# Performance work log

Measured on AMD Instinct MI355X. Metric: run time of the kernel, lower is better.

Reference implementation:

```python
import jax, jax.numpy as jnp
import numpy as np

N, B, H, D = 8, 4, 16, 64   # batch, beam, heads, head_dim
T, S, L = 16, 1024, 1024    # new tokens, prefix len, past len
E = H * D
SCALE = 1.0 / np.sqrt(D).astype(np.float32)


def setup_inputs() -> dict:
    key = jax.random.key(0)
    ks = jax.random.split(key, 10)
    wscale = 1.0 / np.sqrt(E).astype(np.float32)
    return {
        "hidden_states": jax.random.normal(ks[0], (N * B, T, E), jnp.float32),
        "attention_mask": jnp.zeros((N * B, 1, 1, S + L + T), jnp.float32),
        "rel_pos": jax.random.normal(ks[1], (N * B, H, T, S + L + T), jnp.float32) * 0.1,
        "past_prefix_key": jax.random.normal(ks[2], (N, H, S, D), jnp.float32),
        "past_prefix_value": jax.random.normal(ks[3], (N, H, S, D), jnp.float32),
        "past_key": jax.random.normal(ks[4], (N * B, H, L, D), jnp.float32),
        "past_value": jax.random.normal(ks[5], (N * B, H, L, D), jnp.float32),
        "Wq": jax.random.normal(ks[6], (E, E), jnp.float32) * wscale,
        "bq": jnp.zeros((E,), jnp.float32),
        "Wk": jax.random.normal(ks[7], (E, E), jnp.float32) * wscale,
        "bk": jnp.zeros((E,), jnp.float32),
        "Wv": jax.random.normal(ks[8], (E, E), jnp.float32) * wscale,
        "bv": jnp.zeros((E,), jnp.float32),
    }


def _heads(x):
    # (NB, T, E) -> (NB, H, T, D)
    nb, t, _ = x.shape
    return x.reshape(nb, t, H, D).transpose(0, 2, 1, 3)


def reference(hidden_states, attention_mask, rel_pos, past_prefix_key,
              past_prefix_value, past_key, past_value, Wq, bq, Wk, bk, Wv, bv):
    q = _heads(hidden_states @ Wq.T + bq)   # (NB,H,T,D)
    k = _heads(hidden_states @ Wk.T + bk)
    v = _heads(hidden_states @ Wv.T + bv)

    # prefix scores: batch-shared prefix KV, per-beam queries
    q5 = q.reshape(N, B, H, T, D)
    prefix_scores = jnp.einsum('bxhtd,bhsd->bxhts', q5, past_prefix_key)
    prefix_scores = prefix_scores.reshape(N * B, H, T, S) * SCALE

    key_layer = jnp.concatenate([past_key, k], axis=2)      # (NB,H,L+T,D)
    value_layer = jnp.concatenate([past_value, v], axis=2)
    scores = jnp.einsum('bhtd,bhsd->bhts', q, key_layer) * SCALE

    scores = jnp.concatenate([prefix_scores, scores], axis=-1)  # (NB,H,T,S+L+T)
    scores = scores + rel_pos + attention_mask
    probs = jax.nn.softmax(scores, axis=-1)

    prefix_probs = probs[..., :S]
    rest_probs = probs[..., S:]

    prefix_ctx = jnp.einsum('bxhts,bhsd->bxhtd',
                            prefix_probs.reshape(N, B, H, T, S),
                            past_prefix_value).reshape(N * B, H, T, D)
    ctx = prefix_ctx + jnp.einsum('bhts,bhsd->bhtd', rest_probs, value_layer)

    # (NB,H,T,D) -> (NB,T,E)
    return ctx.transpose(0, 2, 1, 3).reshape(N * B, T, E)
```

## Files before the change

kernel.cpp:

```cpp
#include <hip/hip_runtime.h>

#define NH 16
#define NT 16
#define DD 64
#define SS 1024
#define LL 1024
#define TOTK 2064
#define EE 1024
#define NWAVE 8

typedef __attribute__((ext_vector_type(8))) short bf16x8;
typedef __attribute__((ext_vector_type(4))) float f32x4;

__device__ __forceinline__ unsigned short f2bf(float x) {
  union { float f; unsigned u; } v; v.f = x;
  unsigned r = v.u + 0x7fffu + ((v.u >> 16) & 1u);
  return (unsigned short)(r >> 16);
}

__device__ __forceinline__ void dma16(const void* g, void* l) {
  __builtin_amdgcn_global_load_lds(
      (const __attribute__((address_space(1))) unsigned int*)g,
      (__attribute__((address_space(3))) unsigned int*)l, 16, 0, 0);
}

__global__ __launch_bounds__(256)
void proj_kernel(const float* __restrict__ hidden,
                 const float* __restrict__ Wq, const float* __restrict__ bq,
                 const float* __restrict__ Wk, const float* __restrict__ bk,
                 const float* __restrict__ Wv, const float* __restrict__ bv,
                 unsigned short* __restrict__ qws,
                 float* __restrict__ kws, float* __restrict__ vws)
{
  __shared__ alignas(16) unsigned short As[64][72];
  __shared__ alignas(16) unsigned short Bs[64][72];
  const int mtile = blockIdx.x;
  const int ntile = blockIdx.y;
  const int mat = ntile >> 4;
  const int h = ntile & 15;
  const float* Wm = (mat == 0) ? Wq : (mat == 1 ? Wk : Wv);
  const float* bm = (mat == 0) ? bq : (mat == 1 ? bk : bv);
  const int tid = threadIdx.x;
  const int lane = tid & 63, w = tid >> 6;
  const int lr = lane & 15, lg = lane >> 4;
  const int m0 = mtile * 64;

  const f32x4 fz = {0.f, 0.f, 0.f, 0.f};
  f32x4 acc[4];
  #pragma unroll
  for (int j = 0; j < 4; ++j) acc[j] = fz;

  const int srow = tid >> 4, sc4 = tid & 15;
  float4 Ar[4], Br[4];
  #pragma unroll
  for (int it = 0; it < 4; ++it) {
    Ar[it] = *(const float4*)(hidden + (m0 + srow + it * 16) * EE + sc4 * 4);
    Br[it] = *(const float4*)(Wm + (h * 64 + srow + it * 16) * EE + sc4 * 4);
  }

  for (int k0 = 0; k0 < EE; k0 += 64) {
    __syncthreads();
    #pragma unroll
    for (int it = 0; it < 4; ++it) {
      int row = srow + it * 16;
      float4 a = Ar[it], b = Br[it];
      *(ushort4*)(&As[row][sc4 * 4]) = make_ushort4(f2bf(a.x), f2bf(a.y), f2bf(a.z), f2bf(a.w));
      *(ushort4*)(&Bs[row][sc4 * 4]) = make_ushort4(f2bf(b.x), f2bf(b.y), f2bf(b.z), f2bf(b.w));
    }
    __syncthreads();
    int kn = k0 + 64;
    if (kn < EE) {
      #pragma unroll
      for (int it = 0; it < 4; ++it) {
        Ar[it] = *(const float4*)(hidden + (m0 + srow + it * 16) * EE + kn + sc4 * 4);
        Br[it] = *(const float4*)(Wm + (h * 64 + srow + it * 16) * EE + kn + sc4 * 4);
      }
    }
    #pragma unroll
    for (int hh = 0; hh < 2; ++hh) {
      bf16x8 a = *(const bf16x8*)(&As[w * 16 + lr][hh * 32 + lg * 8]);
      #pragma unroll
      for (int dt = 0; dt < 4; ++dt) {
        bf16x8 b = *(const bf16x8*)(&Bs[dt * 16 + lr][hh * 32 + lg * 8]);
        acc[dt] = __builtin_amdgcn_mfma_f32_16x16x32_bf16(a, b, acc[dt], 0, 0, 0);
      }
    }
  }

  #pragma unroll
  for (int dt = 0; dt < 4; ++dt)
    #pragma unroll
    for (int r = 0; r < 4; ++r) {
      int Mrow = m0 + w * 16 + lg * 4 + r;
      int nb = Mrow >> 4, t = Mrow & 15;
      int d = dt * 16 + lr;
      float val = acc[dt][r] + bm[h * 64 + d];
      int oi = ((nb * NH + h) * NT + t) * DD + d;
      if (mat == 0) qws[oi] = f2bf(val);
      else if (mat == 1) kws[oi] = val;
      else vws[oi] = val;
    }
}

__global__ __launch_bounds__(512)
void attn_kernel(const float* __restrict__ mask, const float* __restrict__ rel,
                 const float* __restrict__ ppk, const float* __restrict__ ppv,
                 const float* __restrict__ pk, const float* __restrict__ pv,
                 const unsigned short* __restrict__ qws,
                 const float* __restrict__ kws, const float* __restrict__ vws,
                 float* __restrict__ out)
{
  __shared__ __align__(16) float SB[2 * 2 * 128 * 64];
  __shared__ __align__(16) unsigned short Pb[NWAVE][16][40];

  const int wg = blockIdx.x;
  const int nb = wg >> 4, h = wg & 15;
  const int n = nb >> 2;
  const int tid = threadIdx.x;
  const int lane = tid & 63, w = tid >> 6;
  const int lr = lane & 15, lg = lane >> 4;

  const unsigned short* qbase = qws + ((nb * NH + h) * NT) * DD;
  bf16x8 aq0 = *(const bf16x8*)(qbase + lr * DD + lg * 8);
  bf16x8 aq1 = *(const bf16x8*)(qbase + lr * DD + lg * 8 + 32);

  const float* relbase = rel + ((nb * NH + h) * NT) * TOTK;
  const float* mbase = mask + nb * TOTK;

  if (lane < 32) {
    int t = lane & 15, half = lane >> 4;
    float4 z = {0.f, 0.f, 0.f, 0.f};
    *(float4*)(&Pb[w][t][16 + half * 8]) = z;
  }

  const f32x4 fz = {0.f, 0.f, 0.f, 0.f};
  f32x4 ctx[4];
  float ls[4];
  #pragma unroll
  for (int dt = 0; dt < 4; ++dt) ctx[dt] = fz;
  #pragma unroll
  for (int r = 0; r < 4; ++r) ls[r] = 0.f;

  auto stage = [&](int c, int buf) {
    const float *ks, *vs;
    if (c < 8) {
      int j = c * 128;
      ks = ppk + ((n * NH + h) * SS + j) * DD;
      vs = ppv + ((n * NH + h) * SS + j) * DD;
    } else if (c < 16) {
      int j = (c - 8) * 128;
      ks = pk + ((nb * NH + h) * LL + j) * DD;
      vs = pv + ((nb * NH + h) * LL + j) * DD;
    } else {
      ks = kws + ((nb * NH + h) * NT) * DD;
      vs = vws + ((nb * NH + h) * NT) * DD;
    }
    float* Kb = SB + buf * 2 * 128 * 64;
    float* Vb = Kb + 128 * 64;
    #pragma unroll
    for (int q = 0; q < 4; ++q) {
      int Lrow = w * 16 + q * 4 + (lane >> 4);
      int colb = (lane & 15) * 16;
      int scolb = colb ^ ((Lrow & 7) << 4);
      int srow = (c == 16) ? (Lrow & 15) : Lrow;
      const char* gk = (const char*)ks + srow * 256 + scolb;
      const char* gv = (const char*)vs + srow * 256 + scolb;
      dma16(gk, Kb + (w * 16 + q * 4) * 64);
      dma16(gv, Vb + (w * 16 + q * 4) * 64);
    }
  };

  stage(0, 0);

  for (int c = 0; c < 17; ++c) {
    const int buf = c & 1;
    const int kb0 = c * 128 + w * 16;
    const bool active = kb0 < TOTK;

    float rraw[4]; float mv = 0.f;
    if (active) {
      #pragma unroll
      for (int r = 0; r < 4; ++r)
        rraw[r] = relbase[(lg * 4 + r) * TOTK + kb0 + lr];
      mv = mbase[kb0 + lr];
    }

    if (c < 16) stage(c + 1, buf ^ 1);

    __builtin_amdgcn_sched_barrier(0);
    if (c < 16) asm volatile("s_waitcnt vmcnt(8)" ::: "memory");
    else        asm volatile("s_waitcnt vmcnt(0)" ::: "memory");
    __builtin_amdgcn_sched_barrier(0);

    if (active) {
      const float* Kb = SB + buf * 2 * 128 * 64;
      const float* Vb = Kb + 128 * 64;

      bf16x8 kbf[2];
      #pragma unroll
      for (int hh = 0; hh < 2; ++hh) {
        bf16x8 o;
        #pragma unroll
        for (int q = 0; q < 2; ++q) {
          int colb = (hh * 128 + lg * 32 + q * 16) ^ ((lr & 7) << 4);
          float4 v = *(const float4*)((const char*)Kb + (w * 16 + lr) * 256 + colb);
          o[q * 4 + 0] = (short)f2bf(v.x); o[q * 4 + 1] = (short)f2bf(v.y);
          o[q * 4 + 2] = (short)f2bf(v.z); o[q * 4 + 3] = (short)f2bf(v.w);
        }
        kbf[hh] = o;
      }
      f32x4 s = fz;
      s = __builtin_amdgcn_mfma_f32_16x16x32_bf16(aq0, kbf[0], s, 0, 0, 0);
      s = __builtin_amdgcn_mfma_f32_16x16x32_bf16(aq1, kbf[1], s, 0, 0, 0);

      #pragma unroll
      for (int r = 0; r < 4; ++r) {
        float p = __expf(s[r] * 0.125f + rraw[r] + mv);
        ls[r] += p;
        Pb[w][lg * 4 + r][lr] = f2bf(p);
      }

      bf16x8 pa = *(const bf16x8*)(&Pb[w][lr][lg * 8]);
      #pragma unroll
      for (int dt = 0; dt < 4; ++dt) {
        bf16x8 vb;
        #pragma unroll
        for (int e = 0; e < 8; ++e) {
          int row = lg * 8 + e;
          float vv = 0.f;
          if (row < 16) {
            int colb = ((dt * 16 + lr) * 4) ^ ((row & 7) << 4);
            vv = *(const float*)((const char*)Vb + (w * 16 + row) * 256 + colb);
          }
          vb[e] = (short)f2bf(vv);
        }
        ctx[dt] = __builtin_amdgcn_mfma_f32_16x16x32_bf16(pa, vb, ctx[dt], 0, 0, 0);
      }
    }
  }

  #pragma unroll
  for (int r = 0; r < 4; ++r) {
    #pragma unroll
    for (int o = 8; o >= 1; o >>= 1) ls[r] += __shfl_xor(ls[r], o, 16);
  }

  __syncthreads();
  float* mgc = SB;
  float* mgl = SB + NWAVE * 16 * 64;
  #pragma unroll
  for (int dt = 0; dt < 4; ++dt)
    #pragma unroll
    for (int r = 0; r < 4; ++r)
      mgc[(w * 16 + lg * 4 + r) * 64 + dt * 16 + lr] = ctx[dt][r];
  if (lr == 0) {
    #pragma unroll
    for (int r = 0; r < 4; ++r) mgl[w * 16 + lg * 4 + r] = ls[r];
  }
  __syncthreads();
  #pragma unroll
  for (int i = 0; i < 2; ++i) {
    int idx = i * 512 + tid;
    int t = idx >> 6, d = idx & 63;
    float num = 0.f, den = 0.f;
    #pragma unroll
    for (int ww = 0; ww < NWAVE; ++ww) {
      den += mgl[ww * 16 + t];
      num += mgc[(ww * 16 + t) * 64 + d];
    }
    out[((nb * NT + t) * NH + h) * DD + d] = num / den;
  }
}

extern "C" void kernel_launch(void* const* d_in, const int* in_sizes, int n_in,
                              void* d_out, int out_size, void* d_ws, size_t ws_size,
                              hipStream_t stream) {
  const float* hidden = (const float*)d_in[0];
  const float* mask   = (const float*)d_in[1];
  const float* rel    = (const float*)d_in[2];
  const float* ppk    = (const float*)d_in[3];
  const float* ppv    = (const float*)d_in[4];
  const float* pk     = (const float*)d_in[5];
  const float* pv     = (const float*)d_in[6];
  const float* Wq     = (const float*)d_in[7];
  const float* bq     = (const float*)d_in[8];
  const float* Wk     = (const float*)d_in[9];
  const float* bk     = (const float*)d_in[10];
  const float* Wv     = (const float*)d_in[11];
  const float* bv     = (const float*)d_in[12];
  float* out = (float*)d_out;

  unsigned short* qws = (unsigned short*)d_ws;
  float* kws = (float*)((char*)d_ws + (1u << 20));
  float* vws = (float*)((char*)d_ws + 3u * (1u << 20));

  proj_kernel<<<dim3(8, 48), 256, 0, stream>>>(hidden, Wq, bq, Wk, bk, Wv, bv,
                                               qws, kws, vws);
  attn_kernel<<<dim3(512), 512, 0, stream>>>(mask, rel, ppk, ppv, pk, pv,
                                             qws, kws, vws, out);
}
```

Measured before the change: 117.0 us.

## Stage only K through LDS, load V directly to registers, pair chunks per MFMA

Only K tiles are now DMA'd into shared memory, and the shared buffer is halved. V is loaded straight from global memory into registers, laid out so that each PV MFMA covers two 16-key sub-chunks and the K=32 slot is filled with no zero padding. The main loop now processes chunk pairs with hand-set vmcnt waits, the final 16-token tail is handled by wave 0 alone, and the launch bounds ask for two blocks per CU. The aim is less LDS traffic and footprint plus higher occupancy, at the cost of more registers (32 floats of V per lane) and fragile manual waitcnt accounting.

```diff
diff --git a/kernel.cpp b/kernel.cpp
--- a/kernel.cpp
+++ b/kernel.cpp
@@ -102,7 +102,7 @@
     }
 }
 
-__global__ __launch_bounds__(512)
+__global__ __launch_bounds__(512, 2)
 void attn_kernel(const float* __restrict__ mask, const float* __restrict__ rel,
                  const float* __restrict__ ppk, const float* __restrict__ ppv,
                  const float* __restrict__ pk, const float* __restrict__ pv,
@@ -110,7 +110,7 @@
                  const float* __restrict__ kws, const float* __restrict__ vws,
                  float* __restrict__ out)
 {
-  __shared__ __align__(16) float SB[2 * 2 * 128 * 64];
+  __shared__ __align__(16) float SB[2 * 128 * 64];
   __shared__ __align__(16) unsigned short Pb[NWAVE][16][40];
 
   const int wg = blockIdx.x;
@@ -127,12 +127,6 @@
   const float* relbase = rel + ((nb * NH + h) * NT) * TOTK;
   const float* mbase = mask + nb * TOTK;
 
-  if (lane < 32) {
-    int t = lane & 15, half = lane >> 4;
-    float4 z = {0.f, 0.f, 0.f, 0.f};
-    *(float4*)(&Pb[w][t][16 + half * 8]) = z;
-  }
-
   const f32x4 fz = {0.f, 0.f, 0.f, 0.f};
   f32x4 ctx[4];
   float ls[4];
@@ -141,101 +135,133 @@
   #pragma unroll
   for (int r = 0; r < 4; ++r) ls[r] = 0.f;
 
-  auto stage = [&](int c, int buf) {
-    const float *ks, *vs;
-    if (c < 8) {
-      int j = c * 128;
-      ks = ppk + ((n * NH + h) * SS + j) * DD;
-      vs = ppv + ((n * NH + h) * SS + j) * DD;
-    } else if (c < 16) {
-      int j = (c - 8) * 128;
-      ks = pk + ((nb * NH + h) * LL + j) * DD;
-      vs = pv + ((nb * NH + h) * LL + j) * DD;
-    } else {
-      ks = kws + ((nb * NH + h) * NT) * DD;
-      vs = vws + ((nb * NH + h) * NT) * DD;
-    }
-    float* Kb = SB + buf * 2 * 128 * 64;
-    float* Vb = Kb + 128 * 64;
+  auto kstage = [&](int c, int buf) {
+    const float* ks = (c < 8)  ? ppk + ((n * NH + h) * SS + c * 128) * DD
+                    : (c < 16) ? pk + ((nb * NH + h) * LL + (c - 8) * 128) * DD
+                               : kws + ((nb * NH + h) * NT) * DD;
+    float* Kb = SB + buf * 128 * 64;
     #pragma unroll
     for (int q = 0; q < 4; ++q) {
       int Lrow = w * 16 + q * 4 + (lane >> 4);
       int colb = (lane & 15) * 16;
       int scolb = colb ^ ((Lrow & 7) << 4);
       int srow = (c == 16) ? (Lrow & 15) : Lrow;
-      const char* gk = (const char*)ks + srow * 256 + scolb;
-      const char* gv = (const char*)vs + srow * 256 + scolb;
-      dma16(gk, Kb + (w * 16 + q * 4) * 64);
-      dma16(gv, Vb + (w * 16 + q * 4) * 64);
+      dma16((const char*)ks + srow * 256 + scolb, Kb + (w * 16 + q * 4) * 64);
     }
   };
 
-  stage(0, 0);
-
-  for (int c = 0; c < 17; ++c) {
-    const int buf = c & 1;
-    const int kb0 = c * 128 + w * 16;
-    const bool active = kb0 < TOTK;
-
-    float rraw[4]; float mv = 0.f;
-    if (active) {
-      #pragma unroll
-      for (int r = 0; r < 4; ++r)
-        rraw[r] = relbase[(lg * 4 + r) * TOTK + kb0 + lr];
-      mv = mbase[kb0 + lr];
-    }
-
-    if (c < 16) stage(c + 1, buf ^ 1);
-
-    __builtin_amdgcn_sched_barrier(0);
-    if (c < 16) asm volatile("s_waitcnt vmcnt(8)" ::: "memory");
-    else        asm volatile("s_waitcnt vmcnt(0)" ::: "memory");
-    __builtin_amdgcn_sched_barrier(0);
-
-    if (active) {
-      const float* Kb = SB + buf * 2 * 128 * 64;
-      const float* Vb = Kb + 128 * 64;
-
-      bf16x8 kbf[2];
-      #pragma unroll
-      for (int hh = 0; hh < 2; ++hh) {
-        bf16x8 o;
-        #pragma unroll
-        for (int q = 0; q < 2; ++q) {
-          int colb = (hh * 128 + lg * 32 + q * 16) ^ ((lr & 7) << 4);
-          float4 v = *(const float4*)((const char*)Kb + (w * 16 + lr) * 256 + colb);
-          o[q * 4 + 0] = (short)f2bf(v.x); o[q * 4 + 1] = (short)f2bf(v.y);
-          o[q * 4 + 2] = (short)f2bf(v.z); o[q * 4 + 3] = (short)f2bf(v.w);
-        }
-        kbf[hh] = o;
-      }
-      f32x4 s = fz;
-      s = __builtin_amdgcn_mfma_f32_16x16x32_bf16(aq0, kbf[0], s, 0, 0, 0);
-      s = __builtin_amdgcn_mfma_f32_16x16x32_bf16(aq1, kbf[1], s, 0, 0, 0);
-
-      #pragma unroll
-      for (int r = 0; r < 4; ++r) {
-        float p = __expf(s[r] * 0.125f + rraw[r] + mv);
-        ls[r] += p;
-        Pb[w][lg * 4 + r][lr] = f2bf(p);
-      }
-
-      bf16x8 pa = *(const bf16x8*)(&Pb[w][lr][lg * 8]);
-      #pragma unroll
-      for (int dt = 0; dt < 4; ++dt) {
-        bf16x8 vb;
-        #pragma unroll
-        for (int e = 0; e < 8; ++e) {
-          int row = lg * 8 + e;
-          float vv = 0.f;
-          if (row < 16) {
-            int colb = ((dt * 16 + lr) * 4) ^ ((row & 7) << 4);
-            vv = *(const float*)((const char*)Vb + (w * 16 + row) * 256 + colb);
-          }
-          vb[e] = (short)f2bf(vv);
-        }
-        ctx[dt] = __builtin_amdgcn_mfma_f32_16x16x32_bf16(pa, vb, ctx[dt], 0, 0, 0);
-      }
+  auto qk_sub = [&](const float* Kb, const float rr[4], float mv, int sub) {
+    bf16x8 kbf[2];
+    #pragma unroll
+    for (int hh = 0; hh < 2; ++hh) {
+      bf16x8 o;
+      #pragma unroll
+      for (int q = 0; q < 2; ++q) {
+        int colb = (hh * 128 + lg * 32 + q * 16) ^ ((lr & 7) << 4);
+        float4 v = *(const float4*)((const char*)Kb + (w * 16 + lr) * 256 + colb);
+        o[q * 4 + 0] = (short)f2bf(v.x); o[q * 4 + 1] = (short)f2bf(v.y);
+        o[q * 4 + 2] = (short)f2bf(v.z); o[q * 4 + 3] = (short)f2bf(v.w);
+      }
+      kbf[hh] = o;
+    }
+    f32x4 s = fz;
+    s = __builtin_amdgcn_mfma_f32_16x16x32_bf16(aq0, kbf[0], s, 0, 0, 0);
+    s = __builtin_amdgcn_mfma_f32_16x16x32_bf16(aq1, kbf[1], s, 0, 0, 0);
+    #pragma unroll
+    for (int r = 0; r < 4; ++r) {
+      float p = __expf(s[r] * 0.125f + rr[r] + mv);
+      ls[r] += p;
+      Pb[w][lg * 4 + r][sub * 16 + lr] = f2bf(p);
+    }
+  };
+
+  kstage(0, 0);
+  kstage(1, 1);
+
+  for (int cp = 0; cp < 8; ++cp) {
+    const int cA = 2 * cp;
+    const int kbA = cA * 128 + w * 16;
+    const int kbB = kbA + 128;
+
+    const float* vs = (cp < 4) ? ppv + ((n * NH + h) * SS + cA * 128) * DD
+                               : pv + ((nb * NH + h) * LL + (cA - 8) * 128) * DD;
+    float vraw[32];
+    #pragma unroll
+    for (int dt = 0; dt < 4; ++dt)
+      #pragma unroll
+      for (int e = 0; e < 8; ++e) {
+        int kslot = lg * 8 + e;
+        int j = (kslot >> 4) * 128 + w * 16 + (kslot & 15);
+        vraw[dt * 8 + e] = vs[j * DD + dt * 16 + lr];
+      }
+    float rrA[4], rrB[4];
+    #pragma unroll
+    for (int r = 0; r < 4; ++r) {
+      rrA[r] = relbase[(lg * 4 + r) * TOTK + kbA + lr];
+      rrB[r] = relbase[(lg * 4 + r) * TOTK + kbB + lr];
+    }
+    float mvA = mbase[kbA + lr];
+    float mvB = mbase[kbB + lr];
+
+    __builtin_amdgcn_sched_barrier(0);
+    asm volatile("s_waitcnt vmcnt(46)" ::: "memory");
+    __builtin_amdgcn_sched_barrier(0);
+
+    qk_sub(SB, rrA, mvA, 0);
+
+    __builtin_amdgcn_sched_barrier(0);
+    kstage(cA + 2, 0);
+    __builtin_amdgcn_sched_barrier(0);
+    asm volatile("s_waitcnt vmcnt(46)" ::: "memory");
+    __builtin_amdgcn_sched_barrier(0);
+
+    qk_sub(SB + 128 * 64, rrB, mvB, 1);
+
+    __builtin_amdgcn_sched_barrier(0);
+    if (cp < 7) kstage(cA + 3, 1);
+    __builtin_amdgcn_sched_barrier(0);
+
+    bf16x8 pa = *(const bf16x8*)(&Pb[w][lr][lg * 8]);
+    #pragma unroll
+    for (int dt = 0; dt < 4; ++dt) {
+      bf16x8 vb;
+      #pragma unroll
+      for (int e = 0; e < 8; ++e) vb[e] = (short)f2bf(vraw[dt * 8 + e]);
+      ctx[dt] = __builtin_amdgcn_mfma_f32_16x16x32_bf16(pa, vb, ctx[dt], 0, 0, 0);
+    }
+  }
+
+  if (w == 0) {
+    #pragma unroll
+    for (int r = 0; r < 4; ++r) Pb[0][lg * 4 + r][16 + lr] = 0;
+    const float* vs = vws + ((nb * NH + h) * NT) * DD;
+    float vraw[32];
+    #pragma unroll
+    for (int dt = 0; dt < 4; ++dt)
+      #pragma unroll
+      for (int e = 0; e < 8; ++e) {
+        int kslot = lg * 8 + e;
+        vraw[dt * 8 + e] = (kslot < 16) ? vs[kslot * DD + dt * 16 + lr] : 0.f;
+      }
+    float rrT[4];
+    #pragma unroll
+    for (int r = 0; r < 4; ++r)
+      rrT[r] = relbase[(lg * 4 + r) * TOTK + 2048 + lr];
+    float mvT = mbase[2048 + lr];
+
+    __builtin_amdgcn_sched_barrier(0);
+    asm volatile("s_waitcnt vmcnt(0)" ::: "memory");
+    __builtin_amdgcn_sched_barrier(0);
+
+    qk_sub(SB, rrT, mvT, 0);
+
+    bf16x8 pa = *(const bf16x8*)(&Pb[0][lr][lg * 8]);
+    #pragma unroll
+    for (int dt = 0; dt < 4; ++dt) {
+      bf16x8 vb;
+      #pragma unroll
+      for (int e = 0; e < 8; ++e) vb[e] = (short)f2bf(vraw[dt * 8 + e]);
+      ctx[dt] = __builtin_amdgcn_mfma_f32_16x16x32_bf16(pa, vb, ctx[dt], 0, 0, 0);
     }
   }
 
```

New measurement: 111.1 us. 1.05x faster.
